# Performance work log

Measured on AMD Instinct MI355X. Metric: run time of the kernel, lower is better.

The kernel has to match this reference:

```python
import jax, jax.numpy as jnp
import numpy as np
from jax import lax

NUM_GROUPS = 16
POOL_K = 2
CLAMP_MIN = 0.0
CLAMP_MAX = 1.0
EPS = 1e-5


def setup_inputs() -> dict:
    key = jax.random.key(0)
    k1, k2, k3, k4, k5, k6 = jax.random.split(key, 6)
    B, Cin, H, W = 32, 64, 128, 128
    Cout, K = 128, 3
    x = jax.random.normal(k1, (B, Cin, H, W), dtype=jnp.float32)
    conv_w = jax.random.normal(k2, (Cout, Cin, K, K), dtype=jnp.float32) * 0.05
    conv_b = jax.random.normal(k3, (Cout,), dtype=jnp.float32) * 0.05
    gn_weight = jnp.ones((Cout,), dtype=jnp.float32) + 0.1 * jax.random.normal(k4, (Cout,), dtype=jnp.float32)
    gn_bias = 0.1 * jax.random.normal(k5, (Cout,), dtype=jnp.float32)
    scale = jnp.ones((Cout, 1, 1), dtype=jnp.float32) + 0.1 * jax.random.normal(k6, (Cout, 1, 1), dtype=jnp.float32)
    return {"x": x, "conv_w": conv_w, "conv_b": conv_b,
            "gn_weight": gn_weight, "gn_bias": gn_bias, "scale": scale}


def reference(x, conv_w, conv_b, gn_weight, gn_bias, scale):
    # Conv2d, VALID padding, stride 1  -> [B, C, H-2, W-2]
    y = lax.conv_general_dilated(
        x, conv_w, window_strides=(1, 1), padding='VALID',
        dimension_numbers=('NCHW', 'OIHW', 'NCHW'))
    y = y + conv_b[None, :, None, None]

    B, C, H, W = y.shape
    # GroupNorm: stats per (batch, group) over channels_per_group*H*W
    yg = y.reshape(B, NUM_GROUPS, -1)
    mean = jnp.mean(yg, axis=-1, keepdims=True)
    var = jnp.mean(jnp.square(yg - mean), axis=-1, keepdims=True)
    yn = ((yg - mean) * lax.rsqrt(var + EPS)).reshape(B, C, H, W)
    # affine + extra per-channel scale (fused elementwise)
    yn = (yn * gn_weight[None, :, None, None] + gn_bias[None, :, None, None]) * scale[None]

    # MaxPool2d(k=POOL_K), VALID, stride=k
    p = lax.reduce_window(yn, -jnp.inf, lax.max,
                          (1, 1, POOL_K, POOL_K), (1, 1, POOL_K, POOL_K), 'VALID')
    return jnp.clip(p, CLAMP_MIN, CLAMP_MAX)
```

## Files before the change

kernel.cpp:

```cpp
#include <hip/hip_runtime.h>

typedef _Float16 half8 __attribute__((ext_vector_type(8)));
typedef _Float16 half4t __attribute__((ext_vector_type(4)));
typedef _Float16 half2t __attribute__((ext_vector_type(2)));
typedef float float4t __attribute__((ext_vector_type(4)));
typedef float float4u __attribute__((ext_vector_type(4), aligned(4)));

#define BATCH 32
#define CIN 64
#define HIN 128
#define WIN 128
#define COUT 128
#define HOUT 126
#define WOUT 126
#define HP 63
#define WP 63
#define NGROUPS 16
#define CPG 8
#define EPSV 1e-5f

#define XPR 8320
#define XPRB 16640

__global__ __launch_bounds__(256) void prep_kernel(
    const float* __restrict__ x, const float* __restrict__ w,
    _Float16* __restrict__ xp, _Float16* __restrict__ wT,
    float* __restrict__ stats)
{
    const int tid = threadIdx.x;
    if (blockIdx.x >= 128) {
        const int pos = blockIdx.x - 128;
        const int idx = blockIdx.y * 256 + tid;
        const int cout = idx >> 6, cin = idx & 63;
        wT[pos * (COUT * CIN) + idx] = (_Float16)w[(cout * CIN + cin) * 9 + pos];
        if (blockIdx.x == 128 && blockIdx.y == 0)
            ((float4t*)stats)[tid] = (float4t){0.f, 0.f, 0.f, 0.f};
        return;
    }

    const int grow = blockIdx.x;
    const int b = blockIdx.y;
    const int colq = tid >> 3;
    const int chk  = tid & 7;
    const int c0 = colq * 4;

    const float* xb = x + (((size_t)b * CIN + chk * 8) * HIN + grow) * WIN + c0;
    float4t v[8];
#pragma unroll
    for (int i = 0; i < 8; i++)
        v[i] = *(const float4t*)(xb + (size_t)i * HIN * WIN);

    _Float16* xpb = xp + ((size_t)b * HIN + grow) * XPR;
#pragma unroll
    for (int j = 0; j < 4; j++) {
        int col = c0 + j;
        int slot = chk ^ ((2 * grow + col) & 7);
        half8 h = { (_Float16)v[0][j], (_Float16)v[1][j], (_Float16)v[2][j],
                    (_Float16)v[3][j], (_Float16)v[4][j], (_Float16)v[5][j],
                    (_Float16)v[6][j], (_Float16)v[7][j] };
        *(half8*)(xpb + col * 64 + slot * 8) = h;
    }
    if (tid < 16) {
        int col = 128 + (tid >> 3), ck = tid & 7;
        int slot = ck ^ ((2 * grow + col) & 7);
        half8 z;
#pragma unroll
        for (int j = 0; j < 8; j++) z[j] = (_Float16)0.f;
        *(half8*)(xpb + col * 64 + slot * 8) = z;
    }
}

__global__ __launch_bounds__(256, 2) void conv_mfma_kernel(
    const _Float16* __restrict__ xp, const _Float16* __restrict__ wT,
    const float* __restrict__ bias, unsigned int* __restrict__ pl,
    float* __restrict__ stats)
{
    __shared__ __align__(16) _Float16 xs[4 * XPR];

    const int tid = threadIdx.x;
    int f = blockIdx.y * 63 + blockIdx.x;
    int w = (f & 7) * 252 + (f >> 3);
    const int s = w % 63;
    const int b = w / 63;
    const int oy = 2 * s;

    const int lane = tid & 63;
    const int wv = tid >> 6;
    const int w2 = wv & 1;
    const int nh = wv >> 1;
    const int m = lane & 15;
    const int q = lane >> 4;
    const int cb = w2 * 64;

    {
        const char* src = (const char*)(xp + ((size_t)b * HIN + oy) * XPR);
#pragma unroll
        for (int k = 0; k < 16; k++) {
            int chunk = wv * 16 + k;
            __builtin_amdgcn_global_load_lds(
                (const __attribute__((address_space(1))) void*)(src + chunk * 1024 + lane * 16),
                (__attribute__((address_space(3))) void*)((char*)xs + chunk * 1024), 16, 0, 0);
        }
        if (wv == 0) {
            __builtin_amdgcn_global_load_lds(
                (const __attribute__((address_space(1))) void*)(src + 65536 + lane * 16),
                (__attribute__((address_space(3))) void*)((char*)xs + 65536), 16, 0, 0);
        }
    }

    const _Float16* wBase = wT + (size_t)(cb + m) * CIN + q * 8;

    half8 a[4], na[4], nna[4];
#pragma unroll
    for (int sub = 0; sub < 4; sub++) {
        a[sub]  = *(const half8*)(wBase + (size_t)sub * 16 * CIN);
        na[sub] = *(const half8*)(wBase + (size_t)sub * 16 * CIN + 32);
    }

    float bv[4];
#pragma unroll
    for (int sub = 0; sub < 4; sub++) bv[sub] = bias[cb + sub * 16 + m];

    float4t acc0[4][4], acc1[4][4];
#pragma unroll
    for (int sub = 0; sub < 4; sub++)
#pragma unroll
        for (int n = 0; n < 4; n++) {
            acc0[sub][n] = (float4t){0.f, 0.f, 0.f, 0.f};
            acc1[sub][n] = (float4t){0.f, 0.f, 0.f, 0.f};
        }

    __syncthreads();

#pragma unroll
    for (int kk = 0; kk < 18; kk++) {
        const int pos = kk >> 1, ch = kk & 1;
        const int kh = (pos > 2) + (pos > 5);
        const int kw = pos - kh * 3;
        int key0 = (2 * (oy + kh) + m + kw) & 7;
        int key1 = (key0 + 2) & 7;
        const _Float16* b0 = &xs[kh * XPR + (m + kw) * 64 + (((q + 4 * ch) ^ key0) << 3)];
        const _Float16* b1 = &xs[(kh + 1) * XPR + (m + kw) * 64 + (((q + 4 * ch) ^ key1) << 3)];

        const int nk = (kk < 16) ? kk + 2 : 0;
        const int npos = nk >> 1, nch = nk & 1;
#pragma unroll
        for (int sub = 0; sub < 4; sub++)
            nna[sub] = *(const half8*)(wBase + (size_t)npos * COUT * CIN
                                       + (size_t)sub * 16 * CIN + nch * 32);

        __builtin_amdgcn_s_setprio(1);
#pragma unroll
        for (int n = 0; n < 4; n++) {
            half8 bf0 = *(const half8*)(b0 + (nh * 4 + n) * 1024);
            half8 bf1 = *(const half8*)(b1 + (nh * 4 + n) * 1024);
#pragma unroll
            for (int sub = 0; sub < 4; sub++) {
                acc0[sub][n] = __builtin_amdgcn_mfma_f32_16x16x32_f16(bf0, a[sub], acc0[sub][n], 0, 0, 0);
                acc1[sub][n] = __builtin_amdgcn_mfma_f32_16x16x32_f16(bf1, a[sub], acc1[sub][n], 0, 0, 0);
            }
        }
        __builtin_amdgcn_s_setprio(0);
#pragma unroll
        for (int sub = 0; sub < 4; sub++) { a[sub] = na[sub]; na[sub] = nna[sub]; }
    }

    float sv[4] = {0.f, 0.f, 0.f, 0.f}, ssv[4] = {0.f, 0.f, 0.f, 0.f};
#pragma unroll
    for (int sub = 0; sub < 4; sub++) {
        const int c = cb + sub * 16 + m;
#pragma unroll
        for (int n = 0; n < 4; n++) {
            int pix0 = (nh * 4 + n) * 16 + q * 4;
            float p00 = acc0[sub][n][0] + bv[sub];
            float p01 = acc0[sub][n][1] + bv[sub];
            float p02 = acc0[sub][n][2] + bv[sub];
            float p03 = acc0[sub][n][3] + bv[sub];
            float p10 = acc1[sub][n][0] + bv[sub];
            float p11 = acc1[sub][n][1] + bv[sub];
            float p12 = acc1[sub][n][2] + bv[sub];
            float p13 = acc1[sub][n][3] + bv[sub];
            sv[sub]  += p00 + p01 + p10 + p11;
            ssv[sub] += p00 * p00 + p01 * p01 + p10 * p10 + p11 * p11;
            if (pix0 != 124) {
                sv[sub]  += p02 + p03 + p12 + p13;
                ssv[sub] += p02 * p02 + p03 * p03 + p12 * p12 + p13 * p13;
            }
            float mx0 = fmaxf(fmaxf(p00, p01), fmaxf(p10, p11));
            float mn0 = fminf(fminf(p00, p01), fminf(p10, p11));
            float mx1 = fmaxf(fmaxf(p02, p03), fmaxf(p12, p13));
            float mn1 = fminf(fminf(p02, p03), fminf(p12, p13));
            half4t o = { (_Float16)mx0, (_Float16)mn0, (_Float16)mx1, (_Float16)mn1 };
            unsigned int* dst = pl + (((size_t)b * COUT + c) * HP + s) * 64
                                + (nh * 4 + n) * 8 + 2 * q;
            *(half4t*)dst = o;
        }
    }

#pragma unroll
    for (int sub = 0; sub < 4; sub++) {
        float aa = sv[sub], cc = ssv[sub];
        aa += __shfl_xor(aa, 1);  cc += __shfl_xor(cc, 1);
        aa += __shfl_xor(aa, 2);  cc += __shfl_xor(cc, 2);
        aa += __shfl_xor(aa, 4);  cc += __shfl_xor(cc, 4);
        aa += __shfl_xor(aa, 16); cc += __shfl_xor(cc, 16);
        aa += __shfl_xor(aa, 32); cc += __shfl_xor(cc, 32);
        if ((lane & 55) == 0) {
            int g = w2 * 8 + sub * 2 + ((lane >> 3) & 1);
            atomicAdd(&stats[(b * NGROUPS + g) * 2 + 0], aa);
            atomicAdd(&stats[(b * NGROUPS + g) * 2 + 1], cc);
        }
    }
}

__global__ __launch_bounds__(256) void norm_pool_kernel(
    const unsigned int* __restrict__ pl, const float* __restrict__ stats,
    const float* __restrict__ gnw, const float* __restrict__ gnb,
    const float* __restrict__ scale, float* __restrict__ out)
{
    const int t  = threadIdx.x & 15;
    const int hs = threadIdx.x >> 4;
    const int hblk = blockIdx.x & 3;
    const int c = (blockIdx.x >> 2) & 127;
    const int b = blockIdx.x >> 9;
    const int hp = hblk * 16 + hs;

    const float N = (float)(CPG * HOUT * WOUT);
    int g = c >> 3;
    float sum   = stats[(b * NGROUPS + g) * 2 + 0];
    float sumsq = stats[(b * NGROUPS + g) * 2 + 1];
    float mean = sum / N;
    float var  = sumsq / N - mean * mean;
    float rstd = rsqrtf(var + EPSV);

    float gw = gnw[c] * rstd;
    float A  = gw * scale[c];
    float B2 = (gnb[c] - mean * gw) * scale[c];

    if (hp >= HP) return;

    const unsigned int* yp = pl + (((size_t)b * COUT + c) * HP + hp) * 64 + t * 4;
    half8 rv = *(const half8*)yp;

    float o[4];
#pragma unroll
    for (int j = 0; j < 4; j++) {
        float vx = fmaf((float)rv[2 * j],     A, B2);
        float vn = fmaf((float)rv[2 * j + 1], A, B2);
        float mx = fmaxf(vx, vn);
        o[j] = fminf(fmaxf(mx, 0.0f), 1.0f);
    }

    float* op = out + (((size_t)b * COUT + c) * HP + hp) * WP + t * 4;
    if (t < 15) {
        *(float4u*)op = (float4u){o[0], o[1], o[2], o[3]};
    } else {
        op[0] = o[0]; op[1] = o[1]; op[2] = o[2];
    }
}

extern "C" void kernel_launch(void* const* d_in, const int* in_sizes, int n_in,
                              void* d_out, int out_size, void* d_ws, size_t ws_size,
                              hipStream_t stream) {
    const float* x      = (const float*)d_in[0];
    const float* conv_w = (const float*)d_in[1];
    const float* conv_b = (const float*)d_in[2];
    const float* gnw    = (const float*)d_in[3];
    const float* gnb    = (const float*)d_in[4];
    const float* scale  = (const float*)d_in[5];
    float* out = (float*)d_out;

    const size_t pl_bytes = (size_t)BATCH * COUT * HP * 64 * 4;
    unsigned int* pl = (unsigned int*)d_ws;
    float* stats = (float*)((char*)d_ws + pl_bytes);
    _Float16* wT = (_Float16*)((char*)d_ws + pl_bytes + 4096);
    _Float16* xp = (_Float16*)((char*)d_ws + pl_bytes + 4096 + 147456);

    dim3 pgrid(137, BATCH);
    prep_kernel<<<pgrid, 256, 0, stream>>>(x, conv_w, xp, wT, stats);

    dim3 grid(HP, BATCH);
    conv_mfma_kernel<<<grid, 256, 0, stream>>>(xp, wT, conv_b, pl, stats);

    norm_pool_kernel<<<BATCH * COUT * 4, 256, 0, stream>>>(
        pl, stats, gnw, gnb, scale, out);
}
```

Measured before the change: 340.4 us.

## Split conv tile by output row instead of channel half, combine pool via LDS

Each wave now covers all 128 output channels for one of the two conv rows, where before it covered 64 channels for both rows. This halves the LDS B-fragment reads per MFMA but doubles the weight fragments each wave loads from global memory, and the weight prefetch depth drops from two steps to one. The vertical half of the 2x2 max/min pool now goes through shared memory with two extra barriers between row waves. Register pressure changes (8 weight fragments plus prefetch) and the weaker prefetch could expose global load latency.

```diff
diff --git a/kernel.cpp b/kernel.cpp
--- a/kernel.cpp
+++ b/kernel.cpp
@@ -86,11 +86,10 @@
 
     const int lane = tid & 63;
     const int wv = tid >> 6;
-    const int w2 = wv & 1;
+    const int row = wv & 1;
     const int nh = wv >> 1;
     const int m = lane & 15;
     const int q = lane >> 4;
-    const int cb = w2 * 64;
 
     {
         const char* src = (const char*)(xp + ((size_t)b * HIN + oy) * XPR);
@@ -108,27 +107,23 @@
         }
     }
 
-    const _Float16* wBase = wT + (size_t)(cb + m) * CIN + q * 8;
-
-    half8 a[4], na[4], nna[4];
-#pragma unroll
-    for (int sub = 0; sub < 4; sub++) {
-        a[sub]  = *(const half8*)(wBase + (size_t)sub * 16 * CIN);
-        na[sub] = *(const half8*)(wBase + (size_t)sub * 16 * CIN + 32);
-    }
-
-    float bv[4];
-#pragma unroll
-    for (int sub = 0; sub < 4; sub++) bv[sub] = bias[cb + sub * 16 + m];
-
-    float4t acc0[4][4], acc1[4][4];
-#pragma unroll
-    for (int sub = 0; sub < 4; sub++)
-#pragma unroll
-        for (int n = 0; n < 4; n++) {
-            acc0[sub][n] = (float4t){0.f, 0.f, 0.f, 0.f};
-            acc1[sub][n] = (float4t){0.f, 0.f, 0.f, 0.f};
-        }
+    const _Float16* wBase = wT + (size_t)m * CIN + q * 8;
+
+    half8 a[8], na[8];
+#pragma unroll
+    for (int sub = 0; sub < 8; sub++)
+        a[sub] = *(const half8*)(wBase + (size_t)sub * 16 * CIN);
+
+    float bv[8];
+#pragma unroll
+    for (int sub = 0; sub < 8; sub++) bv[sub] = bias[sub * 16 + m];
+
+    float4t acc[8][4];
+#pragma unroll
+    for (int sub = 0; sub < 8; sub++)
+#pragma unroll
+        for (int n = 0; n < 4; n++)
+            acc[sub][n] = (float4t){0.f, 0.f, 0.f, 0.f};
 
     __syncthreads();
 
@@ -137,68 +132,86 @@
         const int pos = kk >> 1, ch = kk & 1;
         const int kh = (pos > 2) + (pos > 5);
         const int kw = pos - kh * 3;
-        int key0 = (2 * (oy + kh) + m + kw) & 7;
-        int key1 = (key0 + 2) & 7;
-        const _Float16* b0 = &xs[kh * XPR + (m + kw) * 64 + (((q + 4 * ch) ^ key0) << 3)];
-        const _Float16* b1 = &xs[(kh + 1) * XPR + (m + kw) * 64 + (((q + 4 * ch) ^ key1) << 3)];
-
-        const int nk = (kk < 16) ? kk + 2 : 0;
+        int key = (2 * (oy + row + kh) + m + kw) & 7;
+        const _Float16* bb = &xs[(row + kh) * XPR + (m + kw) * 64 + (((q + 4 * ch) ^ key) << 3)];
+
+        const int nk = (kk < 17) ? kk + 1 : 0;
         const int npos = nk >> 1, nch = nk & 1;
 #pragma unroll
-        for (int sub = 0; sub < 4; sub++)
-            nna[sub] = *(const half8*)(wBase + (size_t)npos * COUT * CIN
-                                       + (size_t)sub * 16 * CIN + nch * 32);
+        for (int sub = 0; sub < 8; sub++)
+            na[sub] = *(const half8*)(wBase + (size_t)npos * COUT * CIN
+                                      + (size_t)sub * 16 * CIN + nch * 32);
 
         __builtin_amdgcn_s_setprio(1);
 #pragma unroll
         for (int n = 0; n < 4; n++) {
-            half8 bf0 = *(const half8*)(b0 + (nh * 4 + n) * 1024);
-            half8 bf1 = *(const half8*)(b1 + (nh * 4 + n) * 1024);
-#pragma unroll
-            for (int sub = 0; sub < 4; sub++) {
-                acc0[sub][n] = __builtin_amdgcn_mfma_f32_16x16x32_f16(bf0, a[sub], acc0[sub][n], 0, 0, 0);
-                acc1[sub][n] = __builtin_amdgcn_mfma_f32_16x16x32_f16(bf1, a[sub], acc1[sub][n], 0, 0, 0);
+            half8 bf = *(const half8*)(bb + (nh * 4 + n) * 1024);
+#pragma unroll
+            for (int sub = 0; sub < 8; sub++)
+                acc[sub][n] = __builtin_amdgcn_mfma_f32_16x16x32_f16(bf, a[sub], acc[sub][n], 0, 0, 0);
+        }
+        __builtin_amdgcn_s_setprio(0);
+#pragma unroll
+        for (int sub = 0; sub < 8; sub++) a[sub] = na[sub];
+    }
+
+    float sv[8], ssv[8];
+    half4t hmm[8][4];
+#pragma unroll
+    for (int sub = 0; sub < 8; sub++) { sv[sub] = 0.f; ssv[sub] = 0.f; }
+#pragma unroll
+    for (int sub = 0; sub < 8; sub++) {
+#pragma unroll
+        for (int n = 0; n < 4; n++) {
+            int pix0 = nh * 64 + n * 16 + q * 4;
+            float p0 = acc[sub][n][0] + bv[sub];
+            float p1 = acc[sub][n][1] + bv[sub];
+            float p2 = acc[sub][n][2] + bv[sub];
+            float p3 = acc[sub][n][3] + bv[sub];
+            sv[sub]  += p0 + p1;
+            ssv[sub] += p0 * p0 + p1 * p1;
+            if (pix0 != 124) {
+                sv[sub]  += p2 + p3;
+                ssv[sub] += p2 * p2 + p3 * p3;
             }
-        }
-        __builtin_amdgcn_s_setprio(0);
-#pragma unroll
-        for (int sub = 0; sub < 4; sub++) { a[sub] = na[sub]; na[sub] = nna[sub]; }
-    }
-
-    float sv[4] = {0.f, 0.f, 0.f, 0.f}, ssv[4] = {0.f, 0.f, 0.f, 0.f};
-#pragma unroll
-    for (int sub = 0; sub < 4; sub++) {
-        const int c = cb + sub * 16 + m;
-#pragma unroll
-        for (int n = 0; n < 4; n++) {
-            int pix0 = (nh * 4 + n) * 16 + q * 4;
-            float p00 = acc0[sub][n][0] + bv[sub];
-            float p01 = acc0[sub][n][1] + bv[sub];
-            float p02 = acc0[sub][n][2] + bv[sub];
-            float p03 = acc0[sub][n][3] + bv[sub];
-            float p10 = acc1[sub][n][0] + bv[sub];
-            float p11 = acc1[sub][n][1] + bv[sub];
-            float p12 = acc1[sub][n][2] + bv[sub];
-            float p13 = acc1[sub][n][3] + bv[sub];
-            sv[sub]  += p00 + p01 + p10 + p11;
-            ssv[sub] += p00 * p00 + p01 * p01 + p10 * p10 + p11 * p11;
-            if (pix0 != 124) {
-                sv[sub]  += p02 + p03 + p12 + p13;
-                ssv[sub] += p02 * p02 + p03 * p03 + p12 * p12 + p13 * p13;
+            float mx0 = fmaxf(p0, p1), mn0 = fminf(p0, p1);
+            float mx1 = fmaxf(p2, p3), mn1 = fminf(p2, p3);
+            hmm[sub][n] = (half4t){ (_Float16)mx0, (_Float16)mn0,
+                                    (_Float16)mx1, (_Float16)mn1 };
+        }
+    }
+
+    __syncthreads();
+    half4t* sc = (half4t*)xs;
+    if (row == 1) {
+#pragma unroll
+        for (int sub = 0; sub < 8; sub++)
+#pragma unroll
+            for (int n = 0; n < 4; n++)
+                sc[((nh * 8 + sub) * 4 + n) * 64 + lane] = hmm[sub][n];
+    }
+    __syncthreads();
+    if (row == 0) {
+#pragma unroll
+        for (int sub = 0; sub < 8; sub++) {
+            const int c = sub * 16 + m;
+#pragma unroll
+            for (int n = 0; n < 4; n++) {
+                half4t o2 = sc[((nh * 8 + sub) * 4 + n) * 64 + lane];
+                half4t h = hmm[sub][n];
+                half4t o = { h[0] > o2[0] ? h[0] : o2[0],
+                             h[1] < o2[1] ? h[1] : o2[1],
+                             h[2] > o2[2] ? h[2] : o2[2],
+                             h[3] < o2[3] ? h[3] : o2[3] };
+                unsigned int* dst = pl + (((size_t)b * COUT + c) * HP + s) * 64
+                                    + nh * 32 + n * 8 + 2 * q;
+                *(half4t*)dst = o;
             }
-            float mx0 = fmaxf(fmaxf(p00, p01), fmaxf(p10, p11));
-            float mn0 = fminf(fminf(p00, p01), fminf(p10, p11));
-            float mx1 = fmaxf(fmaxf(p02, p03), fmaxf(p12, p13));
-            float mn1 = fminf(fminf(p02, p03), fminf(p12, p13));
-            half4t o = { (_Float16)mx0, (_Float16)mn0, (_Float16)mx1, (_Float16)mn1 };
-            unsigned int* dst = pl + (((size_t)b * COUT + c) * HP + s) * 64
-                                + (nh * 4 + n) * 8 + 2 * q;
-            *(half4t*)dst = o;
-        }
-    }
-
-#pragma unroll
-    for (int sub = 0; sub < 4; sub++) {
+        }
+    }
+
+#pragma unroll
+    for (int sub = 0; sub < 8; sub++) {
         float aa = sv[sub], cc = ssv[sub];
         aa += __shfl_xor(aa, 1);  cc += __shfl_xor(cc, 1);
         aa += __shfl_xor(aa, 2);  cc += __shfl_xor(cc, 2);
@@ -206,7 +219,7 @@
         aa += __shfl_xor(aa, 16); cc += __shfl_xor(cc, 16);
         aa += __shfl_xor(aa, 32); cc += __shfl_xor(cc, 32);
         if ((lane & 55) == 0) {
-            int g = w2 * 8 + sub * 2 + ((lane >> 3) & 1);
+            int g = sub * 2 + ((lane >> 3) & 1);
             atomicAdd(&stats[(b * NGROUPS + g) * 2 + 0], aa);
             atomicAdd(&stats[(b * NGROUPS + g) * 2 + 1], cc);
         }
```

Result: slower. 461.3 us (+35.5%).
